# Performance work log

Measured on AMD Instinct MI355X. Metric: run time of the kernel, lower is better.

The kernel has to match this reference:

```python
import jax, jax.numpy as jnp
import numpy as np

B, T, N, F_IN, F_OUT, E = 4, 12, 2048, 64, 64, 32768


def setup_inputs() -> dict:
    key = jax.random.key(0)
    ks = jax.random.split(key, 10)
    s = 1.0 / np.sqrt(F_IN)
    return {
        "x": jax.random.normal(ks[0], (B, T, N, F_IN), dtype=jnp.float32),
        "edge_index": jax.random.randint(ks[1], (2, E), 0, N, dtype=jnp.int64),
        "Wk": jax.random.normal(ks[2], (F_IN, F_OUT), dtype=jnp.float32) * s,
        "bk": jax.random.normal(ks[3], (F_OUT,), dtype=jnp.float32) * s,
        "Wq": jax.random.normal(ks[4], (F_IN, F_OUT), dtype=jnp.float32) * s,
        "bq": jax.random.normal(ks[5], (F_OUT,), dtype=jnp.float32) * s,
        "Wv": jax.random.normal(ks[6], (F_IN, F_OUT), dtype=jnp.float32) * s,
        "bv": jax.random.normal(ks[7], (F_OUT,), dtype=jnp.float32) * s,
        "Wskip": jax.random.normal(ks[8], (F_IN, F_OUT), dtype=jnp.float32) * s,
        "bias": jax.random.normal(ks[9], (F_OUT,), dtype=jnp.float32) * s,
    }


def reference(x, edge_index, Wk, bk, Wq, bq, Wv, bv, Wskip, bias):
    b, t, n, _ = x.shape
    xs = x.reshape(b * t, n, -1)                       # (b t) n f
    # per-node projections (small GEMMs)
    k = xs @ Wk + bk                                   # key from target nodes
    q = xs @ Wq + bq                                   # query from source nodes
    v = xs @ Wv + bv                                   # value from source nodes
    src, dst = edge_index[0], edge_index[1]            # j -> i (source_to_target)
    # per-edge gate + message: LeakyReLU(k_i + q_j) * v_j  [(b t), E, f_out]
    msg = jax.nn.leaky_relu(k[:, dst] + q[:, src], negative_slope=0.01) * v[:, src]
    # scatter-add aggregation at target nodes
    agg = jnp.zeros_like(k).at[:, dst].add(msg)
    out = agg + xs @ Wskip + bias
    return out.reshape(b, t, n, -1)
```

## Files before the change

kernel.cpp:

```cpp
#include <hip/hip_runtime.h>
#include <hip/hip_bf16.h>

#define BT 48
#define NN 2048
#define FF 64
#define EE 32768
#define ROWS (BT*NN)

typedef __attribute__((ext_vector_type(8))) short short8v;
typedef __attribute__((ext_vector_type(4))) float float4v;

__device__ __forceinline__ unsigned cvt2(float lo, float hi){
    __hip_bfloat162 h = __float22bfloat162_rn(make_float2(lo, hi));
    union { __hip_bfloat162 h; unsigned u; } c; c.h = h; return c.u;
}

__global__ __launch_bounds__(256) void proj_kernel(
    const float* __restrict__ x,
    const float* __restrict__ Wk, const float* __restrict__ bk,
    const float* __restrict__ Wq, const float* __restrict__ bq,
    const float* __restrict__ Wv, const float* __restrict__ bv,
    const float* __restrict__ Ws, const float* __restrict__ bs,
    float* __restrict__ K, unsigned* __restrict__ QV,
    float* __restrict__ out)
{
    __shared__ float vb[64][65];
    const int tid = threadIdx.x;
    const int w  = tid >> 6;
    const int l  = tid & 63;
    const int lr = l & 15;
    const int lh = l >> 4;
    const float* Wm = (w==0)?Wk:(w==1)?Wq:(w==2)?Wv:Ws;
    const float* bm = (w==0)?bk:(w==1)?bq:(w==2)?bv:bs;

    union Frag { unsigned u[4]; short8v s; };

    Frag bf[4][2];
    #pragma unroll
    for (int c=0;c<4;c++){
        #pragma unroll
        for (int h=0;h<2;h++){
            #pragma unroll
            for (int jj=0;jj<4;jj++){
                const int k0 = h*32 + lh*8 + 2*jj;
                const float w0 = Wm[(size_t)k0*FF     + c*16 + lr];
                const float w1 = Wm[(size_t)(k0+1)*FF + c*16 + lr];
                bf[c][h].u[jj] = cvt2(w0, w1);
            }
        }
    }

    float4v acc[4][4];
    #pragma unroll
    for (int c=0;c<4;c++){
        const float bias = bm[c*16 + lr];
        #pragma unroll
        for (int rt=0;rt<4;rt++) acc[c][rt] = float4v{bias,bias,bias,bias};
    }

    const int row0 = blockIdx.x * 64;
    #pragma unroll
    for (int rt=0;rt<4;rt++){
        const float* xr = x + (size_t)(row0 + rt*16 + lr)*FF + lh*8;
        const float4 xa0 = *(const float4*)(xr);
        const float4 xa1 = *(const float4*)(xr + 4);
        const float4 xb0 = *(const float4*)(xr + 32);
        const float4 xb1 = *(const float4*)(xr + 36);
        Frag a0, a1;
        a0.u[0]=cvt2(xa0.x,xa0.y); a0.u[1]=cvt2(xa0.z,xa0.w);
        a0.u[2]=cvt2(xa1.x,xa1.y); a0.u[3]=cvt2(xa1.z,xa1.w);
        a1.u[0]=cvt2(xb0.x,xb0.y); a1.u[1]=cvt2(xb0.z,xb0.w);
        a1.u[2]=cvt2(xb1.x,xb1.y); a1.u[3]=cvt2(xb1.z,xb1.w);
        #pragma unroll
        for (int c=0;c<4;c++){
            acc[c][rt] = __builtin_amdgcn_mfma_f32_16x16x32_bf16(a0.s, bf[c][0].s, acc[c][rt], 0,0,0);
            acc[c][rt] = __builtin_amdgcn_mfma_f32_16x16x32_bf16(a1.s, bf[c][1].s, acc[c][rt], 0,0,0);
        }
    }

    if (w == 2){
        #pragma unroll
        for (int c=0;c<4;c++)
            #pragma unroll
            for (int rt=0;rt<4;rt++)
                #pragma unroll
                for (int j=0;j<4;j++)
                    vb[rt*16 + lh*4 + j][c*16 + lr] = acc[c][rt][j];
    }
    __syncthreads();

    if (w == 0){
        #pragma unroll
        for (int c=0;c<4;c++)
            #pragma unroll
            for (int rt=0;rt<4;rt++)
                #pragma unroll
                for (int j=0;j<4;j++)
                    K[(size_t)(row0 + rt*16 + lh*4 + j)*FF + c*16 + lr] = acc[c][rt][j];
    } else if (w == 1){
        #pragma unroll
        for (int c=0;c<4;c++)
            #pragma unroll
            for (int rt=0;rt<4;rt++)
                #pragma unroll
                for (int j=0;j<4;j++){
                    const int row = rt*16 + lh*4 + j, col = c*16 + lr;
                    QV[(size_t)(row0 + row)*FF + col] = cvt2(acc[c][rt][j], vb[row][col]);
                }
    } else if (w == 3){
        #pragma unroll
        for (int c=0;c<4;c++)
            #pragma unroll
            for (int rt=0;rt<4;rt++)
                #pragma unroll
                for (int j=0;j<4;j++)
                    out[(size_t)(row0 + rt*16 + lh*4 + j)*FF + c*16 + lr] = acc[c][rt][j];
    }
}

__device__ __forceinline__ void gbar(int* ctr, int nblk){
    __syncthreads();
    if (threadIdx.x == 0){
        __threadfence();
        atomicAdd(ctr, 1);
        while (__hip_atomic_load(ctr, __ATOMIC_ACQUIRE, __HIP_MEMORY_SCOPE_AGENT) < nblk) {}
    }
    __syncthreads();
}

__global__ __launch_bounds__(256) void csr_kernel(
    const unsigned int* __restrict__ ew,
    int* __restrict__ flag, int* __restrict__ bar,
    int* __restrict__ deg, int* __restrict__ offs,
    int* __restrict__ cur, int* __restrict__ elist)
{
    const int t = threadIdx.x, b = blockIdx.x;
    const int gtid = b*256 + t;

    for (int i=gtid; i<NN; i+=16384) deg[i] = 0;
    if (gtid < 16) elist[EE + gtid] = 0;
    unsigned f = 0;
    for (int i=gtid; i<8192; i+=16384) f |= ew[2*i+1];
    if (f) atomicOr((unsigned int*)flag, f);
    gbar(bar+0, 64);
    const bool i64 = (*flag == 0);

    for (int e=gtid; e<EE; e+=16384){
        const int d = i64 ? (int)ew[2*(EE+e)] : (int)ew[EE+e];
        atomicAdd(&deg[d], 1);
    }
    gbar(bar+1, 64);

    if (b == 0){
        __shared__ int wsums[4];
        const int base = t*8;
        int v[8], pre[8];
        #pragma unroll
        for (int j=0;j<8;j++) v[j] = deg[base+j];
        pre[0] = 0;
        #pragma unroll
        for (int j=1;j<8;j++) pre[j] = pre[j-1] + v[j-1];
        const int s = pre[7] + v[7];
        int inc = s;
        const int lane = t & 63, wid = t >> 6;
        #pragma unroll
        for (int d=1; d<64; d<<=1){ int tt = __shfl_up(inc, d, 64); if (lane>=d) inc += tt; }
        if (lane == 63) wsums[wid] = inc;
        __syncthreads();
        if (t == 0){ int a=0; for (int k2=0;k2<4;k2++){ int tt=wsums[k2]; wsums[k2]=a; a+=tt; } }
        __syncthreads();
        const int excl = wsums[wid] + (inc - s);
        #pragma unroll
        for (int j=0;j<8;j++){ offs[base+j] = excl + pre[j]; cur[base+j] = excl + pre[j]; }
        if (t == 255) offs[NN] = excl + s;
    }
    gbar(bar+2, 64);

    for (int e=gtid; e<EE; e+=16384){
        int d, s;
        if (i64){ d = (int)ew[2*(EE+e)]; s = (int)ew[2*e]; }
        else    { d = (int)ew[EE+e];     s = (int)ew[e];   }
        const int pos = atomicAdd(&cur[d], 1);
        elist[pos] = s;
    }
}

#define ACCF(uc, kc, accc) { \
    const float q_ = __uint_as_float((uc) << 16); \
    const float v_ = __uint_as_float((uc) & 0xFFFF0000u); \
    float g_ = (kc) + q_; g_ = fmaxf(g_, 0.01f*g_); \
    (accc) = fmaf(g_, v_, (accc)); }
#define ACCFM(uc, kc, accc, m) { \
    const float q_ = __uint_as_float((uc) << 16); \
    const float v_ = __uint_as_float((uc) & 0xFFFF0000u) * (m); \
    float g_ = (kc) + q_; g_ = fmaxf(g_, 0.01f*g_); \
    (accc) = fmaf(g_, v_, (accc)); }

__global__ __launch_bounds__(256) void agg_kernel(
    const float* __restrict__ K, const unsigned* __restrict__ QV,
    const int* __restrict__ offs, const int* __restrict__ elist,
    float* __restrict__ out)
{
    const int tid  = threadIdx.x;
    const int lane = tid & 63;
    const int w    = tid >> 6;
    const int b    = blockIdx.x;
    const int xcd  = b & 7;
    const int li   = b >> 3;
    const int bt   = xcd*6 + (li >> 9);
    const int node = ((li & 511) << 2) | w;
    const int sub  = lane >> 4;
    const int fq   = lane & 15;
    const size_t S    = (size_t)NN*FF;
    const size_t rowb = (size_t)bt*S + (size_t)node*FF;

    const float4 kf = *(const float4*)(K + rowb + fq*4);
    const unsigned* QVb = QV + (size_t)bt*S;

    float4 acc = {0.f,0.f,0.f,0.f};
    const int s0 = offs[node], s1 = offs[node+1];

    for (int i = s0; i < s1; i += 16){
        const int rem  = s1 - i;
        const int base = i + 4*sub;
        const int e0 = elist[base+0];
        const int e1 = elist[base+1];
        const int e2 = elist[base+2];
        const int e3 = elist[base+3];
        const uint4 u0 = *(const uint4*)(QVb + (((unsigned)e0)<<6) + (fq<<2));
        const uint4 u1 = *(const uint4*)(QVb + (((unsigned)e1)<<6) + (fq<<2));
        const uint4 u2 = *(const uint4*)(QVb + (((unsigned)e2)<<6) + (fq<<2));
        const uint4 u3 = *(const uint4*)(QVb + (((unsigned)e3)<<6) + (fq<<2));
        if (rem >= 16){
            ACCF(u0.x, kf.x, acc.x); ACCF(u0.y, kf.y, acc.y);
            ACCF(u0.z, kf.z, acc.z); ACCF(u0.w, kf.w, acc.w);
            ACCF(u1.x, kf.x, acc.x); ACCF(u1.y, kf.y, acc.y);
            ACCF(u1.z, kf.z, acc.z); ACCF(u1.w, kf.w, acc.w);
            ACCF(u2.x, kf.x, acc.x); ACCF(u2.y, kf.y, acc.y);
            ACCF(u2.z, kf.z, acc.z); ACCF(u2.w, kf.w, acc.w);
            ACCF(u3.x, kf.x, acc.x); ACCF(u3.y, kf.y, acc.y);
            ACCF(u3.z, kf.z, acc.z); ACCF(u3.w, kf.w, acc.w);
        } else {
            const float m0 = (4*sub+0 < rem) ? 1.f : 0.f;
            const float m1 = (4*sub+1 < rem) ? 1.f : 0.f;
            const float m2 = (4*sub+2 < rem) ? 1.f : 0.f;
            const float m3 = (4*sub+3 < rem) ? 1.f : 0.f;
            ACCFM(u0.x, kf.x, acc.x, m0); ACCFM(u0.y, kf.y, acc.y, m0);
            ACCFM(u0.z, kf.z, acc.z, m0); ACCFM(u0.w, kf.w, acc.w, m0);
            ACCFM(u1.x, kf.x, acc.x, m1); ACCFM(u1.y, kf.y, acc.y, m1);
            ACCFM(u1.z, kf.z, acc.z, m1); ACCFM(u1.w, kf.w, acc.w, m1);
            ACCFM(u2.x, kf.x, acc.x, m2); ACCFM(u2.y, kf.y, acc.y, m2);
            ACCFM(u2.z, kf.z, acc.z, m2); ACCFM(u2.w, kf.w, acc.w, m2);
            ACCFM(u3.x, kf.x, acc.x, m3); ACCFM(u3.y, kf.y, acc.y, m3);
            ACCFM(u3.z, kf.z, acc.z, m3); ACCFM(u3.w, kf.w, acc.w, m3);
        }
    }

    acc.x += __shfl_xor(acc.x, 16, 64); acc.y += __shfl_xor(acc.y, 16, 64);
    acc.z += __shfl_xor(acc.z, 16, 64); acc.w += __shfl_xor(acc.w, 16, 64);
    acc.x += __shfl_xor(acc.x, 32, 64); acc.y += __shfl_xor(acc.y, 32, 64);
    acc.z += __shfl_xor(acc.z, 32, 64); acc.w += __shfl_xor(acc.w, 32, 64);

    if (sub == 0){
        const float4 sk = *(const float4*)(out + rowb + fq*4);
        float4 r;
        r.x = acc.x + sk.x; r.y = acc.y + sk.y;
        r.z = acc.z + sk.z; r.w = acc.w + sk.w;
        *(float4*)(out + rowb + fq*4) = r;
    }
}

extern "C" void kernel_launch(void* const* d_in, const int* in_sizes, int n_in,
                              void* d_out, int out_size, void* d_ws, size_t ws_size,
                              hipStream_t stream)
{
    const float* x  = (const float*)d_in[0];
    const unsigned int* ew = (const unsigned int*)d_in[1];
    const float* Wk = (const float*)d_in[2];
    const float* bk = (const float*)d_in[3];
    const float* Wq = (const float*)d_in[4];
    const float* bq = (const float*)d_in[5];
    const float* Wv = (const float*)d_in[6];
    const float* bv = (const float*)d_in[7];
    const float* Ws = (const float*)d_in[8];
    const float* bs = (const float*)d_in[9];
    float* out = (float*)d_out;

    float* K = (float*)d_ws;
    const size_t n = (size_t)ROWS*FF;
    unsigned* QV = (unsigned*)(K + n);
    int* meta  = (int*)(QV + n);
    int* flag  = meta;
    int* bar   = meta + 4;
    int* deg   = meta + 16;
    int* offs  = deg + NN;
    int* cur   = offs + NN + 16;
    int* elist = cur + NN;

    hipMemsetAsync(meta, 0, 32, stream);

    hipLaunchKernelGGL(proj_kernel, dim3(ROWS/64), dim3(256), 0, stream,
                       x, Wk,bk, Wq,bq, Wv,bv, Ws,bs, K, QV, out);
    hipLaunchKernelGGL(csr_kernel, dim3(64), dim3(256), 0, stream,
                       ew, flag, bar, deg, offs, cur, elist);
    hipLaunchKernelGGL(agg_kernel, dim3(ROWS/4), dim3(256), 0, stream,
                       K, QV, offs, elist, out);
}
```

Before: 111.9 us.

## Switch projections and edge aggregation to fp16 packed math, store K as fp16

Moves the projection MFMAs from bf16 to fp16 with transposed operands, so each lane holds four consecutive output columns. The epilogue stores directly and interleaves Q/V without the shared-memory staging buffer and barrier. K is stored as fp16, halving its write and read traffic. The per-edge gate and message math runs in packed half2 arithmetic with fp16 accumulators, cutting ALU work but risking precision loss and overflow in the accumulation for high-degree nodes.

```diff
diff --git a/kernel.cpp b/kernel.cpp
--- a/kernel.cpp
+++ b/kernel.cpp
@@ -1,5 +1,4 @@
 #include <hip/hip_runtime.h>
-#include <hip/hip_bf16.h>
 
 #define BT 48
 #define NN 2048
@@ -7,12 +6,17 @@
 #define EE 32768
 #define ROWS (BT*NN)
 
-typedef __attribute__((ext_vector_type(8))) short short8v;
+typedef __attribute__((ext_vector_type(2))) _Float16 half2v;
+typedef __attribute__((ext_vector_type(8))) _Float16 half8v;
 typedef __attribute__((ext_vector_type(4))) float float4v;
 
-__device__ __forceinline__ unsigned cvt2(float lo, float hi){
-    __hip_bfloat162 h = __float22bfloat162_rn(make_float2(lo, hi));
-    union { __hip_bfloat162 h; unsigned u; } c; c.h = h; return c.u;
+__device__ __forceinline__ unsigned cvt2h(float lo, float hi){
+    union { half2v h; unsigned u; } c;
+    c.h = half2v{(_Float16)lo, (_Float16)hi};
+    return c.u;
+}
+__device__ __forceinline__ half2v h2(unsigned u){
+    union { unsigned u; half2v h; } c; c.u = u; return c.h;
 }
 
 __global__ __launch_bounds__(256) void proj_kernel(
@@ -21,10 +25,9 @@
     const float* __restrict__ Wq, const float* __restrict__ bq,
     const float* __restrict__ Wv, const float* __restrict__ bv,
     const float* __restrict__ Ws, const float* __restrict__ bs,
-    float* __restrict__ K, unsigned* __restrict__ QV,
+    unsigned* __restrict__ Kh, unsigned* __restrict__ QV,
     float* __restrict__ out)
 {
-    __shared__ float vb[64][65];
     const int tid = threadIdx.x;
     const int w  = tid >> 6;
     const int l  = tid & 63;
@@ -33,29 +36,26 @@
     const float* Wm = (w==0)?Wk:(w==1)?Wq:(w==2)?Wv:Ws;
     const float* bm = (w==0)?bk:(w==1)?bq:(w==2)?bv:bs;
 
-    union Frag { unsigned u[4]; short8v s; };
-
-    Frag bf[4][2];
-    #pragma unroll
-    for (int c=0;c<4;c++){
-        #pragma unroll
-        for (int h=0;h<2;h++){
+    union FragH { unsigned u[4]; half8v h; };
+
+    FragH af[4][2];
+    #pragma unroll
+    for (int ft=0;ft<4;ft++)
+        #pragma unroll
+        for (int h=0;h<2;h++)
             #pragma unroll
             for (int jj=0;jj<4;jj++){
                 const int k0 = h*32 + lh*8 + 2*jj;
-                const float w0 = Wm[(size_t)k0*FF     + c*16 + lr];
-                const float w1 = Wm[(size_t)(k0+1)*FF + c*16 + lr];
-                bf[c][h].u[jj] = cvt2(w0, w1);
+                af[ft][h].u[jj] = cvt2h(Wm[(size_t)k0*FF + ft*16 + lr],
+                                        Wm[(size_t)(k0+1)*FF + ft*16 + lr]);
             }
-        }
-    }
 
     float4v acc[4][4];
     #pragma unroll
-    for (int c=0;c<4;c++){
-        const float bias = bm[c*16 + lr];
-        #pragma unroll
-        for (int rt=0;rt<4;rt++) acc[c][rt] = float4v{bias,bias,bias,bias};
+    for (int ft=0;ft<4;ft++){
+        const float4 bv4 = *(const float4*)(bm + ft*16 + lh*4);
+        #pragma unroll
+        for (int rt=0;rt<4;rt++) acc[ft][rt] = float4v{bv4.x,bv4.y,bv4.z,bv4.w};
     }
 
     const int row0 = blockIdx.x * 64;
@@ -66,55 +66,38 @@
         const float4 xa1 = *(const float4*)(xr + 4);
         const float4 xb0 = *(const float4*)(xr + 32);
         const float4 xb1 = *(const float4*)(xr + 36);
-        Frag a0, a1;
-        a0.u[0]=cvt2(xa0.x,xa0.y); a0.u[1]=cvt2(xa0.z,xa0.w);
-        a0.u[2]=cvt2(xa1.x,xa1.y); a0.u[3]=cvt2(xa1.z,xa1.w);
-        a1.u[0]=cvt2(xb0.x,xb0.y); a1.u[1]=cvt2(xb0.z,xb0.w);
-        a1.u[2]=cvt2(xb1.x,xb1.y); a1.u[3]=cvt2(xb1.z,xb1.w);
-        #pragma unroll
-        for (int c=0;c<4;c++){
-            acc[c][rt] = __builtin_amdgcn_mfma_f32_16x16x32_bf16(a0.s, bf[c][0].s, acc[c][rt], 0,0,0);
-            acc[c][rt] = __builtin_amdgcn_mfma_f32_16x16x32_bf16(a1.s, bf[c][1].s, acc[c][rt], 0,0,0);
+        FragH b0, b1;
+        b0.u[0]=cvt2h(xa0.x,xa0.y); b0.u[1]=cvt2h(xa0.z,xa0.w);
+        b0.u[2]=cvt2h(xa1.x,xa1.y); b0.u[3]=cvt2h(xa1.z,xa1.w);
+        b1.u[0]=cvt2h(xb0.x,xb0.y); b1.u[1]=cvt2h(xb0.z,xb0.w);
+        b1.u[2]=cvt2h(xb1.x,xb1.y); b1.u[3]=cvt2h(xb1.z,xb1.w);
+        #pragma unroll
+        for (int ft=0;ft<4;ft++){
+            acc[ft][rt] = __builtin_amdgcn_mfma_f32_16x16x32_f16(af[ft][0].h, b0.h, acc[ft][rt], 0,0,0);
+            acc[ft][rt] = __builtin_amdgcn_mfma_f32_16x16x32_f16(af[ft][1].h, b1.h, acc[ft][rt], 0,0,0);
         }
     }
 
-    if (w == 2){
-        #pragma unroll
-        for (int c=0;c<4;c++)
-            #pragma unroll
-            for (int rt=0;rt<4;rt++)
-                #pragma unroll
-                for (int j=0;j<4;j++)
-                    vb[rt*16 + lh*4 + j][c*16 + lr] = acc[c][rt][j];
-    }
-    __syncthreads();
-
-    if (w == 0){
-        #pragma unroll
-        for (int c=0;c<4;c++)
-            #pragma unroll
-            for (int rt=0;rt<4;rt++)
-                #pragma unroll
-                for (int j=0;j<4;j++)
-                    K[(size_t)(row0 + rt*16 + lh*4 + j)*FF + c*16 + lr] = acc[c][rt][j];
-    } else if (w == 1){
-        #pragma unroll
-        for (int c=0;c<4;c++)
-            #pragma unroll
-            for (int rt=0;rt<4;rt++)
-                #pragma unroll
-                for (int j=0;j<4;j++){
-                    const int row = rt*16 + lh*4 + j, col = c*16 + lr;
-                    QV[(size_t)(row0 + row)*FF + col] = cvt2(acc[c][rt][j], vb[row][col]);
-                }
-    } else if (w == 3){
-        #pragma unroll
-        for (int c=0;c<4;c++)
-            #pragma unroll
-            for (int rt=0;rt<4;rt++)
-                #pragma unroll
-                for (int j=0;j<4;j++)
-                    out[(size_t)(row0 + rt*16 + lh*4 + j)*FF + c*16 + lr] = acc[c][rt][j];
+    #pragma unroll
+    for (int ft=0;ft<4;ft++){
+        const int p0 = ft*8 + lh*2;
+        #pragma unroll
+        for (int rt=0;rt<4;rt++){
+            const size_t row = (size_t)(row0 + rt*16 + lr);
+            const float4v a = acc[ft][rt];
+            if (w == 0){
+                uint2 st; st.x = cvt2h(a[0],a[1]); st.y = cvt2h(a[2],a[3]);
+                *(uint2*)(Kh + row*32 + p0) = st;
+            } else if (w == 1){
+                QV[row*FF + 2*p0]     = cvt2h(a[0],a[1]);
+                QV[row*FF + 2*(p0+1)] = cvt2h(a[2],a[3]);
+            } else if (w == 2){
+                QV[row*FF + 2*p0 + 1]     = cvt2h(a[0],a[1]);
+                QV[row*FF + 2*(p0+1) + 1] = cvt2h(a[2],a[3]);
+            } else {
+                *(float4*)(out + row*FF + ft*16 + lh*4) = make_float4(a[0],a[1],a[2],a[3]);
+            }
+        }
     }
 }
 
@@ -185,19 +168,23 @@
     }
 }
 
-#define ACCF(uc, kc, accc) { \
-    const float q_ = __uint_as_float((uc) << 16); \
-    const float v_ = __uint_as_float((uc) & 0xFFFF0000u); \
-    float g_ = (kc) + q_; g_ = fmaxf(g_, 0.01f*g_); \
-    (accc) = fmaf(g_, v_, (accc)); }
-#define ACCFM(uc, kc, accc, m) { \
-    const float q_ = __uint_as_float((uc) << 16); \
-    const float v_ = __uint_as_float((uc) & 0xFFFF0000u) * (m); \
-    float g_ = (kc) + q_; g_ = fmaxf(g_, 0.01f*g_); \
-    (accc) = fmaf(g_, v_, (accc)); }
+#define HEDGE(U) { \
+    half2v g01 = k01 + h2((U).x); \
+    g01 = __builtin_elementwise_max(g01, g01*c001); \
+    acc01 += g01 * h2((U).y); \
+    half2v g23 = k23 + h2((U).z); \
+    g23 = __builtin_elementwise_max(g23, g23*c001); \
+    acc23 += g23 * h2((U).w); }
+#define HEDGEM(U, M) { \
+    half2v g01 = k01 + h2((U).x); \
+    g01 = __builtin_elementwise_max(g01, g01*c001); \
+    acc01 += g01 * (h2((U).y) * (M)); \
+    half2v g23 = k23 + h2((U).z); \
+    g23 = __builtin_elementwise_max(g23, g23*c001); \
+    acc23 += g23 * (h2((U).w) * (M)); }
 
 __global__ __launch_bounds__(256) void agg_kernel(
-    const float* __restrict__ K, const unsigned* __restrict__ QV,
+    const unsigned* __restrict__ Kh, const unsigned* __restrict__ QV,
     const int* __restrict__ offs, const int* __restrict__ elist,
     float* __restrict__ out)
 {
@@ -211,13 +198,16 @@
     const int node = ((li & 511) << 2) | w;
     const int sub  = lane >> 4;
     const int fq   = lane & 15;
-    const size_t S    = (size_t)NN*FF;
-    const size_t rowb = (size_t)bt*S + (size_t)node*FF;
-
-    const float4 kf = *(const float4*)(K + rowb + fq*4);
+    const size_t S = (size_t)NN*FF;
+
+    const uint2 ku = *(const uint2*)(Kh + ((size_t)bt*NN + node)*32 + 2*fq);
+    const half2v k01 = h2(ku.x), k23 = h2(ku.y);
+    const half2v c001 = half2v{(_Float16)0.01f, (_Float16)0.01f};
+    const half2v one2 = half2v{(_Float16)1.f, (_Float16)1.f};
+    const half2v zero2 = half2v{(_Float16)0.f, (_Float16)0.f};
     const unsigned* QVb = QV + (size_t)bt*S;
 
-    float4 acc = {0.f,0.f,0.f,0.f};
+    half2v acc01 = zero2, acc23 = zero2;
     const int s0 = offs[node], s1 = offs[node+1];
 
     for (int i = s0; i < s1; i += 16){
@@ -232,29 +222,18 @@
         const uint4 u2 = *(const uint4*)(QVb + (((unsigned)e2)<<6) + (fq<<2));
         const uint4 u3 = *(const uint4*)(QVb + (((unsigned)e3)<<6) + (fq<<2));
         if (rem >= 16){
-            ACCF(u0.x, kf.x, acc.x); ACCF(u0.y, kf.y, acc.y);
-            ACCF(u0.z, kf.z, acc.z); ACCF(u0.w, kf.w, acc.w);
-            ACCF(u1.x, kf.x, acc.x); ACCF(u1.y, kf.y, acc.y);
-            ACCF(u1.z, kf.z, acc.z); ACCF(u1.w, kf.w, acc.w);
-            ACCF(u2.x, kf.x, acc.x); ACCF(u2.y, kf.y, acc.y);
-            ACCF(u2.z, kf.z, acc.z); ACCF(u2.w, kf.w, acc.w);
-            ACCF(u3.x, kf.x, acc.x); ACCF(u3.y, kf.y, acc.y);
-            ACCF(u3.z, kf.z, acc.z); ACCF(u3.w, kf.w, acc.w);
+            HEDGE(u0); HEDGE(u1); HEDGE(u2); HEDGE(u3);
         } else {
-            const float m0 = (4*sub+0 < rem) ? 1.f : 0.f;
-            const float m1 = (4*sub+1 < rem) ? 1.f : 0.f;
-            const float m2 = (4*sub+2 < rem) ? 1.f : 0.f;
-            const float m3 = (4*sub+3 < rem) ? 1.f : 0.f;
-            ACCFM(u0.x, kf.x, acc.x, m0); ACCFM(u0.y, kf.y, acc.y, m0);
-            ACCFM(u0.z, kf.z, acc.z, m0); ACCFM(u0.w, kf.w, acc.w, m0);
-            ACCFM(u1.x, kf.x, acc.x, m1); ACCFM(u1.y, kf.y, acc.y, m1);
-            ACCFM(u1.z, kf.z, acc.z, m1); ACCFM(u1.w, kf.w, acc.w, m1);
-            ACCFM(u2.x, kf.x, acc.x, m2); ACCFM(u2.y, kf.y, acc.y, m2);
-            ACCFM(u2.z, kf.z, acc.z, m2); ACCFM(u2.w, kf.w, acc.w, m2);
-            ACCFM(u3.x, kf.x, acc.x, m3); ACCFM(u3.y, kf.y, acc.y, m3);
-            ACCFM(u3.z, kf.z, acc.z, m3); ACCFM(u3.w, kf.w, acc.w, m3);
+            const half2v m0 = (4*sub+0 < rem) ? one2 : zero2;
+            const half2v m1 = (4*sub+1 < rem) ? one2 : zero2;
+            const half2v m2 = (4*sub+2 < rem) ? one2 : zero2;
+            const half2v m3 = (4*sub+3 < rem) ? one2 : zero2;
+            HEDGEM(u0, m0); HEDGEM(u1, m1); HEDGEM(u2, m2); HEDGEM(u3, m3);
         }
     }
+
+    float4 acc = make_float4((float)acc01[0], (float)acc01[1],
+                             (float)acc23[0], (float)acc23[1]);
 
     acc.x += __shfl_xor(acc.x, 16, 64); acc.y += __shfl_xor(acc.y, 16, 64);
     acc.z += __shfl_xor(acc.z, 16, 64); acc.w += __shfl_xor(acc.w, 16, 64);
@@ -262,6 +241,7 @@
     acc.z += __shfl_xor(acc.z, 32, 64); acc.w += __shfl_xor(acc.w, 32, 64);
 
     if (sub == 0){
+        const size_t rowb = ((size_t)bt*NN + node)*FF;
         const float4 sk = *(const float4*)(out + rowb + fq*4);
         float4 r;
         r.x = acc.x + sk.x; r.y = acc.y + sk.y;
@@ -286,9 +266,9 @@
     const float* bs = (const float*)d_in[9];
     float* out = (float*)d_out;
 
-    float* K = (float*)d_ws;
     const size_t n = (size_t)ROWS*FF;
-    unsigned* QV = (unsigned*)(K + n);
+    unsigned* Kh = (unsigned*)d_ws;
+    unsigned* QV = Kh + (size_t)ROWS*32;
     int* meta  = (int*)(QV + n);
     int* flag  = meta;
     int* bar   = meta + 4;
@@ -300,9 +280,9 @@
     hipMemsetAsync(meta, 0, 32, stream);
 
     hipLaunchKernelGGL(proj_kernel, dim3(ROWS/64), dim3(256), 0, stream,
-                       x, Wk,bk, Wq,bq, Wv,bv, Ws,bs, K, QV, out);
+                       x, Wk,bk, Wq,bq, Wv,bv, Ws,bs, Kh, QV, out);
     hipLaunchKernelGGL(csr_kernel, dim3(64), dim3(256), 0, stream,
                        ew, flag, bar, deg, offs, cur, elist);
     hipLaunchKernelGGL(agg_kernel, dim3(ROWS/4), dim3(256), 0, stream,
-                       K, QV, offs, elist, out);
-}
+                       Kh, QV, offs, elist, out);
+}
```

Measured after the change: 107.1 us. 1.04x faster.
